# Optimization experiments

Measured on AMD Instinct MI355X. Metric: run time of the kernel, lower is better.

Reference implementation:

```python
import jax, jax.numpy as jnp
import numpy as np

EPS = 1e-8
TEMPERATURE = 1.0


def setup_inputs() -> dict:
    key = jax.random.key(0)
    basin_seq = jax.random.normal(key, (4, 512, 64), dtype=jnp.float32)
    residual_scale = jnp.ones((), dtype=jnp.float32)  # nn.Parameter(torch.tensor(1.0))
    return {"basin_seq": basin_seq, "residual_scale": residual_scale}


def _project_to_simplex(x):
    sp = jax.nn.softplus(x)
    p = sp / (sp.sum(axis=-1, keepdims=True) + EPS)
    return jnp.maximum(p, EPS)


def _qfi_attention_weights(x, temperature):
    # x: (B, T, D)
    p = _project_to_simplex(x)
    # fisher_rao_distance_simplex re-normalizes both operands
    p = p / (p.sum(axis=-1, keepdims=True) + EPS)
    # Faithful: eps is inside the sqrt, so this is a true (B,T,T,D) reduction,
    # not sqrt(p) @ sqrt(p)^T.
    inner = jnp.sqrt(p[:, :, None, :] * p[:, None, :, :] + EPS).sum(axis=-1)  # (B,T,T)
    inner = jnp.clip(inner, -1.0 + 1e-6, 1.0 - 1e-6)
    dist = 2.0 * jnp.arccos(inner)
    logits = -dist / max(float(temperature), 1e-6)
    return jax.nn.softmax(logits, axis=-1)  # (B,T,T)


def _phi_from_activations(acts):
    # acts: (B, T, D)
    t = acts.shape[1]
    x = acts - acts.mean(axis=1, keepdims=True)
    cov = jnp.einsum('btd,bte->bde', x, x) / (t + EPS)
    var = jnp.maximum(jnp.diagonal(cov, axis1=-2, axis2=-1), EPS)  # (B,D)
    denom = jnp.maximum(jnp.sqrt(var[:, :, None] * var[:, None, :]), EPS)
    corr = jnp.clip(cov / denom, -1.0, 1.0)
    d = corr.shape[-1]
    offdiag = corr * (1.0 - jnp.eye(d, dtype=corr.dtype))
    return jnp.abs(offdiag).mean(axis=(-2, -1))  # (B,)


def _kappa_proxy(x):
    return jnp.linalg.norm(x, axis=-1).mean(axis=-1)  # (B,)


def reference(basin_seq, residual_scale):
    x = basin_seq
    for _ in range(2):
        w = _qfi_attention_weights(x, TEMPERATURE)
        x_attn = jnp.einsum('bij,bjd->bid', w, x)
        x = 0.5 * x + 0.5 * x_attn
        x = x + 0.01 * residual_scale * (x_attn - x)
    phi = _phi_from_activations(x)
    kappa = _kappa_proxy(x)
    return (x, phi, kappa)
```

## Files before the change

### kernel.cpp

```cpp
#include <hip/hip_runtime.h>
#include <math.h>

#define B_ 4
#define T_ 512
#define D_ 64
#define EPS 1e-8f

__device__ __forceinline__ float wave_sum(float v) {
#pragma unroll
  for (int m = 1; m < 64; m <<= 1) v += __shfl_xor(v, m, 64);
  return v;
}
__device__ __forceinline__ float softplus_f(float x) {
  return fmaxf(x, 0.0f) + log1pf(expf(-fabsf(x)));
}

#define DOT4(ACC, A, Bv) \
  ACC = fmaf((A).x, (Bv).x, fmaf((A).y, (Bv).y, fmaf((A).z, (Bv).z, fmaf((A).w, (Bv).w, ACC))))

__global__ __launch_bounds__(256) void proj_kernel(const float* __restrict__ x,
                                                   float* __restrict__ s) {
  int wave = threadIdx.x >> 6, lane = threadIdx.x & 63;
  int row = blockIdx.x * 4 + wave;
  float sp = softplus_f(x[row * D_ + lane]);
  float s1 = wave_sum(sp);
  float p = sp / (s1 + EPS);
  p = fmaxf(p, EPS);
  float s2 = wave_sum(p);
  s[row * D_ + lane] = sqrtf(p / (s2 + EPS));
}

__device__ __forceinline__ void stage512(const float* __restrict__ g,
                                         float* __restrict__ lds, int tid) {
#pragma unroll
  for (int h = 0; h < 2; ++h) {
    float4 v[8];
#pragma unroll
    for (int r = 0; r < 8; ++r) {
      int slot = (h * 8 + r) * 512 + tid;
      int j = slot >> 4, c4 = slot & 15;
      v[r] = *(const float4*)(g + j * 64 + ((c4 ^ ((j >> 2) & 7)) << 2));
    }
#pragma unroll
    for (int r = 0; r < 8; ++r) {
      int slot = (h * 8 + r) * 512 + tid;
      int j = slot >> 4, c4 = slot & 15;
      *(float4*)(lds + j * 64 + (c4 << 2)) = v[r];
    }
  }
}

template <int WRITE_S, int DO_COV>
__global__ __launch_bounds__(512) void fiter_kernel(
    const float* __restrict__ s_g, const float* __restrict__ x_g,
    const float* __restrict__ rsp, float* __restrict__ xout,
    float* __restrict__ sout, float* __restrict__ covp,
    float* __restrict__ meanp, float* __restrict__ kappap) {
  int b = blockIdx.y, i0 = blockIdx.x * 8;
  int tid = threadIdx.x;
  int w = tid >> 6, lane = tid & 63;
  const float* sb = s_g + (size_t)b * (T_ * D_);
  const float* xb = x_g + (size_t)b * (T_ * D_);

  __shared__ __align__(16) float sx[512 * 64];
  __shared__ __align__(16) float wlds[8 * 516];
  __shared__ __align__(16) float redv[8 * 68];
  __shared__ float redM[8][8];
  __shared__ float redS[8][8];
  __shared__ float t8[8][68];
  __shared__ float kred8[8];

  stage512(sb, sx, tid);
  __syncthreads();

  int i4 = lane >> 4, j16 = lane & 15;
  int ia0 = i0 + 2 * i4;
  const float* A0 = sx + ia0 * 64;
  const float* A1 = A0 + 64;
  int mA0 = (ia0 >> 2) & 7, mA1 = ((ia0 + 1) >> 2) & 7;
  const float* Bp = sx + (w * 64 + 4 * j16) * 64;
  int mB = j16 & 7;

  float acc[2][4];
#pragma unroll
  for (int r = 0; r < 2; ++r)
#pragma unroll
    for (int c = 0; c < 4; ++c) acc[r][c] = 0.f;

#pragma unroll
  for (int d4 = 0; d4 < 16; ++d4) {
    float4 a0 = *(const float4*)(A0 + ((d4 ^ mA0) << 2));
    float4 a1 = *(const float4*)(A1 + ((d4 ^ mA1) << 2));
    int ob = (d4 ^ mB) << 2;
    float4 b0 = *(const float4*)(Bp + ob);
    float4 b1 = *(const float4*)(Bp + 64 + ob);
    float4 b2 = *(const float4*)(Bp + 128 + ob);
    float4 b3 = *(const float4*)(Bp + 192 + ob);
    DOT4(acc[0][0], a0, b0); DOT4(acc[0][1], a0, b1);
    DOT4(acc[0][2], a0, b2); DOT4(acc[0][3], a0, b3);
    DOT4(acc[1][0], a1, b0); DOT4(acc[1][1], a1, b1);
    DOT4(acc[1][2], a1, b2); DOT4(acc[1][3], a1, b3);
  }

  float S[2][4];
#pragma unroll
  for (int r = 0; r < 2; ++r)
#pragma unroll
    for (int c = 0; c < 4; ++c) {
      float inner = fminf(fmaxf(acc[r][c], -1.0f + 1e-6f), 1.0f - 1e-6f);
      S[r][c] = -2.0f * acosf(inner);
    }

  float m0 = fmaxf(fmaxf(S[0][0], S[0][1]), fmaxf(S[0][2], S[0][3]));
  float m1 = fmaxf(fmaxf(S[1][0], S[1][1]), fmaxf(S[1][2], S[1][3]));
#pragma unroll
  for (int mm = 1; mm < 16; mm <<= 1) {
    m0 = fmaxf(m0, __shfl_xor(m0, mm, 64));
    m1 = fmaxf(m1, __shfl_xor(m1, mm, 64));
  }
  if (j16 == 0) { redM[2 * i4][w] = m0; redM[2 * i4 + 1][w] = m1; }
  __syncthreads();

  stage512(xb, sx, tid);

  float M0 = redM[2 * i4][0], M1 = redM[2 * i4 + 1][0];
#pragma unroll
  for (int q = 1; q < 8; ++q) {
    M0 = fmaxf(M0, redM[2 * i4][q]);
    M1 = fmaxf(M1, redM[2 * i4 + 1][q]);
  }
  float e[2][4];
  float sl0 = 0.f, sl1 = 0.f;
#pragma unroll
  for (int c = 0; c < 4; ++c) {
    e[0][c] = __expf(S[0][c] - M0); sl0 += e[0][c];
    e[1][c] = __expf(S[1][c] - M1); sl1 += e[1][c];
  }
#pragma unroll
  for (int mm = 1; mm < 16; mm <<= 1) {
    sl0 += __shfl_xor(sl0, mm, 64);
    sl1 += __shfl_xor(sl1, mm, 64);
  }
  if (j16 == 0) { redS[2 * i4][w] = sl0; redS[2 * i4 + 1][w] = sl1; }
  int wb = w * 64 + 4 * j16;
#pragma unroll
  for (int r = 0; r < 2; ++r)
#pragma unroll
    for (int c = 0; c < 4; ++c) wlds[(2 * i4 + r) * 516 + wb + c] = e[r][c];
  __syncthreads();

  int js = tid & 15, dg = (tid >> 4) & 15, ig = tid >> 8;
  int xcol = ((dg ^ (js & 7)) << 2);
  float pacc[4][4];
#pragma unroll
  for (int ii = 0; ii < 4; ++ii)
#pragma unroll
    for (int k = 0; k < 4; ++k) pacc[ii][k] = 0.f;

#pragma unroll 2
  for (int jj = 0; jj < 8; ++jj) {
    int jbase = jj * 64 + js * 4;
    const float* xr = sx + jbase * 64 + xcol;
    float4 x0 = *(const float4*)(xr);
    float4 x1 = *(const float4*)(xr + 64);
    float4 x2 = *(const float4*)(xr + 128);
    float4 x3 = *(const float4*)(xr + 192);
#pragma unroll
    for (int ii = 0; ii < 4; ++ii) {
      float4 wv = *(const float4*)(wlds + (4 * ig + ii) * 516 + jbase);
      pacc[ii][0] = fmaf(wv.x, x0.x, fmaf(wv.y, x1.x, fmaf(wv.z, x2.x, fmaf(wv.w, x3.x, pacc[ii][0]))));
      pacc[ii][1] = fmaf(wv.x, x0.y, fmaf(wv.y, x1.y, fmaf(wv.z, x2.y, fmaf(wv.w, x3.y, pacc[ii][1]))));
      pacc[ii][2] = fmaf(wv.x, x0.z, fmaf(wv.y, x1.z, fmaf(wv.z, x2.z, fmaf(wv.w, x3.z, pacc[ii][2]))));
      pacc[ii][3] = fmaf(wv.x, x0.w, fmaf(wv.y, x1.w, fmaf(wv.z, x2.w, fmaf(wv.w, x3.w, pacc[ii][3]))));
    }
  }
#pragma unroll
  for (int ii = 0; ii < 4; ++ii)
#pragma unroll
    for (int k = 0; k < 4; ++k) {
      float v = pacc[ii][k];
      v += __shfl_xor(v, 1, 64);
      v += __shfl_xor(v, 2, 64);
      v += __shfl_xor(v, 4, 64);
      v += __shfl_xor(v, 8, 64);
      pacc[ii][k] = v;
    }
  if (js == 0) {
#pragma unroll
    for (int ii = 0; ii < 4; ++ii)
      *(float4*)(redv + (4 * ig + ii) * 68 + (dg << 2)) =
          make_float4(pacc[ii][0], pacc[ii][1], pacc[ii][2], pacc[ii][3]);
  }
  __syncthreads();

  {
    int row = w, d = lane;
    float ssum = 0.f;
#pragma unroll
    for (int q = 0; q < 8; ++q) ssum += redS[row][q];
    float xa = redv[row * 68 + d] / ssum;
    int ir = i0 + row;
    int mr = (ir >> 2) & 7;
    float xv = sx[ir * 64 + (((d >> 2) ^ mr) << 2) + (d & 3)];
    float c01 = 0.01f * rsp[0];
    float xn = 0.5f * (1.0f - c01) * xv + 0.5f * (1.0f + c01) * xa;
    size_t gi = ((size_t)(b * T_) + ir) * D_ + d;
    xout[gi] = xn;
    if (WRITE_S) {
      float sp = softplus_f(xn);
      float s1 = wave_sum(sp);
      float p = sp / (s1 + EPS);
      p = fmaxf(p, EPS);
      float s2 = wave_sum(p);
      sout[gi] = sqrtf(p / (s2 + EPS));
    }
    if (DO_COV) {
      t8[row][d] = xn;
      float ksq = wave_sum(xn * xn);
      if (lane == 0) kred8[row] = sqrtf(ksq);
    }
  }

  if (DO_COV) {
    __syncthreads();
    int blk = b * 64 + blockIdx.x;
    int dd = tid >> 3, e8 = tid & 7;
    float ca[8];
#pragma unroll
    for (int k = 0; k < 8; ++k) ca[k] = 0.f;
#pragma unroll
    for (int r = 0; r < 8; ++r) {
      float xd = t8[r][dd];
      float4 v0 = *(const float4*)&t8[r][e8 * 8];
      float4 v1 = *(const float4*)&t8[r][e8 * 8 + 4];
      ca[0] = fmaf(xd, v0.x, ca[0]); ca[1] = fmaf(xd, v0.y, ca[1]);
      ca[2] = fmaf(xd, v0.z, ca[2]); ca[3] = fmaf(xd, v0.w, ca[3]);
      ca[4] = fmaf(xd, v1.x, ca[4]); ca[5] = fmaf(xd, v1.y, ca[5]);
      ca[6] = fmaf(xd, v1.z, ca[6]); ca[7] = fmaf(xd, v1.w, ca[7]);
    }
    float* cp = covp + (size_t)blk * 4096 + dd * 64 + e8 * 8;
    *(float4*)(cp) = make_float4(ca[0], ca[1], ca[2], ca[3]);
    *(float4*)(cp + 4) = make_float4(ca[4], ca[5], ca[6], ca[7]);
    if (tid < 64) {
      float ms = 0.f;
#pragma unroll
      for (int r = 0; r < 8; ++r) ms += t8[r][tid];
      meanp[blk * 64 + tid] = ms;
    }
    if (tid == 0) {
      float ks = 0.f;
#pragma unroll
      for (int r = 0; r < 8; ++r) ks += kred8[r];
      kappap[blk] = ks;
    }
  }
}

__global__ __launch_bounds__(1024) void finalize_kernel(
    const float* __restrict__ covp, const float* __restrict__ meanp,
    const float* __restrict__ kappap, float* __restrict__ out) {
  int b = blockIdx.x, tid = threadIdx.x;
  __shared__ float mu[64];
  __shared__ float var[64];
  __shared__ float phired[16];
  if (tid < 64) {
    float m = 0.f;
#pragma unroll
    for (int s = 0; s < 64; ++s) m += meanp[(b * 64 + s) * 64 + tid];
    mu[tid] = m * (1.0f / 512.0f);
  }
  __syncthreads();

  int dd = tid >> 4, e4 = tid & 15;
  float acc[4] = {0.f, 0.f, 0.f, 0.f};
#pragma unroll
  for (int s = 0; s < 64; ++s) {
    float4 v = *(const float4*)(covp + (size_t)(b * 64 + s) * 4096 + dd * 64 + e4 * 4);
    acc[0] += v.x; acc[1] += v.y; acc[2] += v.z; acc[3] += v.w;
  }
  float mud = mu[dd];
#pragma unroll
  for (int k = 0; k < 4; ++k)
    acc[k] = acc[k] * (1.0f / 512.0f) - mud * mu[e4 * 4 + k];
  if (e4 == (dd >> 2)) var[dd] = fmaxf(acc[dd & 3], EPS);
  __syncthreads();

  float vd = var[dd];
  float psum = 0.f;
#pragma unroll
  for (int k = 0; k < 4; ++k) {
    int e = e4 * 4 + k;
    if (e == dd) continue;
    float denom = fmaxf(sqrtf(vd * var[e]), EPS);
    float cc = fminf(fmaxf(acc[k] / denom, -1.0f), 1.0f);
    psum += fabsf(cc);
  }
  psum = wave_sum(psum);
  if ((tid & 63) == 0) phired[tid >> 6] = psum;
  __syncthreads();
  if (tid == 0) {
    float ph = 0.f;
#pragma unroll
    for (int q = 0; q < 16; ++q) ph += phired[q];
    out[B_ * T_ * D_ + b] = ph * (1.0f / 4096.0f);
    float ks = 0.f;
#pragma unroll
    for (int s = 0; s < 64; ++s) ks += kappap[b * 64 + s];
    out[B_ * T_ * D_ + B_ + b] = ks * (1.0f / 512.0f);
  }
}

extern "C" void kernel_launch(void* const* d_in, const int* in_sizes, int n_in,
                              void* d_out, int out_size, void* d_ws, size_t ws_size,
                              hipStream_t stream) {
  const float* x0 = (const float*)d_in[0];
  const float* rs = (const float*)d_in[1];
  float* out = (float*)d_out;
  float* s0    = (float*)d_ws;
  float* s1    = s0 + B_ * T_ * D_;
  float* x1    = s1 + B_ * T_ * D_;
  float* covp  = x1 + B_ * T_ * D_;
  float* meanp = covp + 256 * 4096;
  float* kappap = meanp + 256 * 64;

  dim3 fgrd(64, 4);
  proj_kernel<<<(B_ * T_) / 4, 256, 0, stream>>>(x0, s0);
  fiter_kernel<1, 0><<<fgrd, 512, 0, stream>>>(s0, x0, rs, x1, s1, (float*)0,
                                               (float*)0, (float*)0);
  fiter_kernel<0, 1><<<fgrd, 512, 0, stream>>>(s1, x1, rs, out, (float*)0, covp,
                                               meanp, kappap);
  finalize_kernel<<<4, 1024, 0, stream>>>(covp, meanp, kappap, out);
}
```

Before: 99.76 us.

## Split covariance finalize across 16 blocks per batch with atomic phi accumulation

```diff
diff --git a/kernel.cpp b/kernel.cpp
--- a/kernel.cpp
+++ b/kernel.cpp
@@ -55,7 +55,8 @@
     const float* __restrict__ s_g, const float* __restrict__ x_g,
     const float* __restrict__ rsp, float* __restrict__ xout,
     float* __restrict__ sout, float* __restrict__ covp,
-    float* __restrict__ meanp, float* __restrict__ kappap) {
+    float* __restrict__ meanp, float* __restrict__ diagp,
+    float* __restrict__ kappap) {
   int b = blockIdx.y, i0 = blockIdx.x * 8;
   int tid = threadIdx.x;
   int w = tid >> 6, lane = tid & 63;
@@ -69,6 +70,8 @@
   __shared__ float redS[8][8];
   __shared__ float t8[8][68];
   __shared__ float kred8[8];
+
+  if (DO_COV && blockIdx.x == 0 && tid == 0) xout[B_ * T_ * D_ + b] = 0.f;
 
   stage512(sb, sx, tid);
   __syncthreads();
@@ -241,6 +244,7 @@
     float* cp = covp + (size_t)blk * 4096 + dd * 64 + e8 * 8;
     *(float4*)(cp) = make_float4(ca[0], ca[1], ca[2], ca[3]);
     *(float4*)(cp + 4) = make_float4(ca[4], ca[5], ca[6], ca[7]);
+    if (e8 == (dd >> 3)) diagp[blk * 64 + dd] = ca[dd & 7];
     if (tid < 64) {
       float ms = 0.f;
 #pragma unroll
@@ -256,57 +260,58 @@
   }
 }
 
-__global__ __launch_bounds__(1024) void finalize_kernel(
+__global__ __launch_bounds__(256) void finalize_kernel(
     const float* __restrict__ covp, const float* __restrict__ meanp,
-    const float* __restrict__ kappap, float* __restrict__ out) {
-  int b = blockIdx.x, tid = threadIdx.x;
-  __shared__ float mu[64];
-  __shared__ float var[64];
-  __shared__ float phired[16];
+    const float* __restrict__ diagp, const float* __restrict__ kappap,
+    float* __restrict__ out) {
+  int g = blockIdx.x, b = blockIdx.y, tid = threadIdx.x;
+  __shared__ float mred[4][64], dred[4][64];
+  __shared__ float mu[64], var[64];
+  __shared__ float phired[4];
+  {
+    int d = tid & 63, q = tid >> 6;
+    float ms = 0.f, ds = 0.f;
+#pragma unroll
+    for (int s = 0; s < 16; ++s) {
+      int sl = q * 16 + s;
+      ms += meanp[(b * 64 + sl) * 64 + d];
+      ds += diagp[(b * 64 + sl) * 64 + d];
+    }
+    mred[q][d] = ms; dred[q][d] = ds;
+  }
+  __syncthreads();
   if (tid < 64) {
-    float m = 0.f;
-#pragma unroll
-    for (int s = 0; s < 64; ++s) m += meanp[(b * 64 + s) * 64 + tid];
-    mu[tid] = m * (1.0f / 512.0f);
-  }
-  __syncthreads();
-
-  int dd = tid >> 4, e4 = tid & 15;
-  float acc[4] = {0.f, 0.f, 0.f, 0.f};
-#pragma unroll
-  for (int s = 0; s < 64; ++s) {
-    float4 v = *(const float4*)(covp + (size_t)(b * 64 + s) * 4096 + dd * 64 + e4 * 4);
-    acc[0] += v.x; acc[1] += v.y; acc[2] += v.z; acc[3] += v.w;
-  }
-  float mud = mu[dd];
-#pragma unroll
-  for (int k = 0; k < 4; ++k)
-    acc[k] = acc[k] * (1.0f / 512.0f) - mud * mu[e4 * 4 + k];
-  if (e4 == (dd >> 2)) var[dd] = fmaxf(acc[dd & 3], EPS);
-  __syncthreads();
-
-  float vd = var[dd];
+    float m = (mred[0][tid] + mred[1][tid] + mred[2][tid] + mred[3][tid]) *
+              (1.0f / 512.0f);
+    float dsum = dred[0][tid] + dred[1][tid] + dred[2][tid] + dred[3][tid];
+    mu[tid] = m;
+    var[tid] = fmaxf(dsum * (1.0f / 512.0f) - m * m, EPS);
+  }
+  __syncthreads();
+
+  int cell = g * 256 + tid;
+  int dd = cell >> 6, e = cell & 63;
+  float csum = 0.f;
+#pragma unroll 4
+  for (int s = 0; s < 64; ++s) csum += covp[(size_t)(b * 64 + s) * 4096 + cell];
+  float cov = csum * (1.0f / 512.0f) - mu[dd] * mu[e];
   float psum = 0.f;
-#pragma unroll
-  for (int k = 0; k < 4; ++k) {
-    int e = e4 * 4 + k;
-    if (e == dd) continue;
-    float denom = fmaxf(sqrtf(vd * var[e]), EPS);
-    float cc = fminf(fmaxf(acc[k] / denom, -1.0f), 1.0f);
-    psum += fabsf(cc);
+  if (e != dd) {
+    float denom = fmaxf(sqrtf(var[dd] * var[e]), EPS);
+    psum = fabsf(fminf(fmaxf(cov / denom, -1.0f), 1.0f));
   }
   psum = wave_sum(psum);
   if ((tid & 63) == 0) phired[tid >> 6] = psum;
   __syncthreads();
   if (tid == 0) {
-    float ph = 0.f;
-#pragma unroll
-    for (int q = 0; q < 16; ++q) ph += phired[q];
-    out[B_ * T_ * D_ + b] = ph * (1.0f / 4096.0f);
-    float ks = 0.f;
-#pragma unroll
-    for (int s = 0; s < 64; ++s) ks += kappap[b * 64 + s];
-    out[B_ * T_ * D_ + B_ + b] = ks * (1.0f / 512.0f);
+    atomicAdd(&out[B_ * T_ * D_ + b],
+              (phired[0] + phired[1] + phired[2] + phired[3]) * (1.0f / 4096.0f));
+    if (g == 0) {
+      float ks = 0.f;
+#pragma unroll
+      for (int s = 0; s < 64; ++s) ks += kappap[b * 64 + s];
+      out[B_ * T_ * D_ + B_ + b] = ks * (1.0f / 512.0f);
+    }
   }
 }
 
@@ -321,13 +326,15 @@
   float* x1    = s1 + B_ * T_ * D_;
   float* covp  = x1 + B_ * T_ * D_;
   float* meanp = covp + 256 * 4096;
-  float* kappap = meanp + 256 * 64;
+  float* diagp = meanp + 256 * 64;
+  float* kappap = diagp + 256 * 64;
 
   dim3 fgrd(64, 4);
   proj_kernel<<<(B_ * T_) / 4, 256, 0, stream>>>(x0, s0);
   fiter_kernel<1, 0><<<fgrd, 512, 0, stream>>>(s0, x0, rs, x1, s1, (float*)0,
-                                               (float*)0, (float*)0);
+                                               (float*)0, (float*)0, (float*)0);
   fiter_kernel<0, 1><<<fgrd, 512, 0, stream>>>(s1, x1, rs, out, (float*)0, covp,
-                                               meanp, kappap);
-  finalize_kernel<<<4, 1024, 0, stream>>>(covp, meanp, kappap, out);
-}
+                                               meanp, diagp, kappap);
+  finalize_kernel<<<dim3(16, B_), 256, 0, stream>>>(covp, meanp, diagp, kappap,
+                                                    out);
+}
```

New measurement: 92.26 us. 7.5% less time.
